# Kernel tuning notes

Hardware: AMD Instinct MI355X
Metric: run time of the kernel (lower is better)

Reference implementation:

```python
import jax, jax.numpy as jnp
import numpy as np

B, T, D_IN, D_OUT = 2, 2048, 2048, 2048
H, KV = 32, 8
HD = D_OUT // H          # 64
G = H // KV              # group_size = 4
ROPE_BASE = 10000.0


def setup_inputs() -> dict:
    key = jax.random.key(0)
    ks = jax.random.split(key, 5)
    s = 0.02  # weight init scale
    return {
        "x":  jax.random.normal(ks[0], (B, T, D_IN), jnp.float32),
        "Wq": jax.random.normal(ks[1], (D_IN, D_OUT), jnp.float32) * s,
        "Wk": jax.random.normal(ks[2], (D_IN, KV * HD), jnp.float32) * s,
        "Wv": jax.random.normal(ks[3], (D_IN, KV * HD), jnp.float32) * s,
        "Wo": jax.random.normal(ks[4], (D_OUT, D_OUT), jnp.float32) * s,
    }


def _rope_cos_sin(t, hd):
    inv = 1.0 / (ROPE_BASE ** (jnp.arange(0, hd, 2, dtype=jnp.float32) / hd))
    ang = jnp.arange(t, dtype=jnp.float32)[:, None] * inv[None, :]  # (T, hd/2)
    return jnp.cos(ang), jnp.sin(ang)


def _apply_rope(x, cos, sin):
    # x: (b, h, T, hd); rotate adjacent pairs (complex multiply, Llama-style)
    xr = x.reshape(x.shape[:-1] + (HD // 2, 2))
    x0, x1 = xr[..., 0], xr[..., 1]
    c = cos[None, None]  # (1,1,T,hd/2)
    s = sin[None, None]
    o0 = x0 * c - x1 * s
    o1 = x0 * s + x1 * c
    return jnp.stack([o0, o1], axis=-1).reshape(x.shape)


def reference(x, Wq, Wk, Wv, Wo):
    b, t, _ = x.shape
    q = (x @ Wq).reshape(b, t, H, HD).transpose(0, 2, 1, 3)    # (b,H,T,hd)
    k = (x @ Wk).reshape(b, t, KV, HD).transpose(0, 2, 1, 3)   # (b,KV,T,hd)
    v = (x @ Wv).reshape(b, t, KV, HD).transpose(0, 2, 1, 3)
    cos, sin = _rope_cos_sin(t, HD)
    q = _apply_rope(q, cos, sin)
    k = _apply_rope(k, cos, sin)
    # GQA: expand KV groups to all heads (repeat_interleave on head dim)
    k = jnp.repeat(k, G, axis=1)  # (b,H,T,hd)
    v = jnp.repeat(v, G, axis=1)
    scores = jnp.einsum('bhqd,bhkd->bhqk', q, k) / jnp.sqrt(jnp.float32(HD))
    causal = jnp.triu(jnp.ones((t, t), dtype=bool), 1)
    scores = jnp.where(causal[None, None], -jnp.inf, scores)
    w = jax.nn.softmax(scores, axis=-1)
    ctx = jnp.einsum('bhqk,bhkd->bqhd', w, v).reshape(b, t, D_OUT)
    return ctx @ Wo
```

## Files before the change

### kernel.cpp

```cpp
#include <hip/hip_runtime.h>

#define TQ 2048
#define NB 2
#define NH 32
#define NKV 8
#define HD 64
#define DIN 2048
#define DOUT 2048
#define NQKV 3072
#define QK_W 2560
#define GK 2048

typedef unsigned short u16;
typedef unsigned int u32;
typedef __attribute__((ext_vector_type(8))) short bf16x8;
typedef __attribute__((ext_vector_type(4))) float f32x4;
typedef __attribute__((ext_vector_type(4))) u16 u16x4;

typedef __attribute__((address_space(1))) const u32 gas_u32;
typedef __attribute__((address_space(3))) u32 las_u32;

#define NEG (-1.0e30f)
#define CL2 0.18033688f

__device__ __forceinline__ u16 f2bf(float f) {
  u32 u = __float_as_uint(f);
  u += 0x7fffu + ((u >> 16) & 1u);
  return (u16)(u >> 16);
}
__device__ __forceinline__ float bf2f(u16 h) { return __uint_as_float(((u32)h) << 16); }
__device__ __forceinline__ u32 cvtpk(float lo, float hi) {
  u32 r;
  asm("v_cvt_pk_bf16_f32 %0, %1, %2" : "=v"(r) : "v"(lo), "v"(hi));
  return r;
}
__device__ __forceinline__ float exp2g(float x) {
  float r;
  asm("v_exp_f32 %0, %1\n\ts_nop 0" : "=v"(r) : "v"(x));
  return r;
}

__global__ __launch_bounds__(256)
void k_cvt(const float* __restrict__ src, u16* __restrict__ dst, int n4) {
  int i = blockIdx.x * 256 + threadIdx.x;
  if (i >= n4) return;
  f32x4 v = *(const f32x4*)(src + (size_t)i * 4);
  u16x4 o;
  o[0] = f2bf(v[0]); o[1] = f2bf(v[1]); o[2] = f2bf(v[2]); o[3] = f2bf(v[3]);
  *(u16x4*)(dst + (size_t)i * 4) = o;
}

__global__ __launch_bounds__(256)
void k_transpose(const float* __restrict__ src, int nsrc, u16* __restrict__ dst, int row0) {
  __shared__ float tile[32][33];
  const int nTK = GK / 32;
  int kt = blockIdx.x % nTK, nt = blockIdx.x / nTK;
  int k0 = kt * 32, n0 = nt * 32;
  int rr = threadIdx.x >> 5, cc = threadIdx.x & 31;
#pragma unroll
  for (int p = 0; p < 4; ++p) {
    int kl = p * 8 + rr;
    tile[kl][cc] = src[(size_t)(k0 + kl) * nsrc + n0 + cc];
  }
  __syncthreads();
#pragma unroll
  for (int p = 0; p < 4; ++p) {
    int nl = p * 8 + rr;
    dst[(size_t)(row0 + n0 + nl) * GK + k0 + cc] = f2bf(tile[cc][nl]);
  }
}

__global__ __launch_bounds__(256)
void k_rope_table(float2* __restrict__ tab) {
  int idx = blockIdx.x * 256 + threadIdx.x;
  int t = idx >> 5, i = idx & 31;
  float inv = 1.0f / powf(10000.0f, (float)i / 32.0f);
  float ang = (float)t * inv;
  tab[idx] = make_float2(cosf(ang), sinf(ang));
}

template <int MODE>
__global__ __launch_bounds__(256, 2)
void k_gemm(const u16* __restrict__ A, const u16* __restrict__ Bt,
            u16* __restrict__ QKV, u16* __restrict__ Vt, float* __restrict__ Cf,
            const float2* __restrict__ tab, int N) {
  __shared__ __align__(16) u16 lds[2][16384];
  const int tid = threadIdx.x;
  const int lane = tid & 63, wid = tid >> 6;
  const int nTN = N >> 7;
  const int tm = blockIdx.x / nTN, tn = blockIdx.x % nTN;
  const int m0 = tm << 7, n0 = tn << 7;
  const int l15 = lane & 15, lg = lane >> 4;
  const int wr = (wid >> 1) << 6, wc = (wid & 1) << 6;

  f32x4 acc[4][4] = {};

  auto stage = [&](int buf, int k0) {
    u16* base = &lds[buf][0];
#pragma unroll
    for (int p = 0; p < 4; ++p) {
      int c = p * 256 + tid;
      int row = c >> 3, kb = c & 7;
      int ksrc = k0 + ((kb ^ (row & 7)) << 3);
      const u16* sA = A + (size_t)(m0 + row) * GK + ksrc;
      __builtin_amdgcn_global_load_lds((gas_u32*)sA, (las_u32*)(base + c * 8), 16, 0, 0);
      const u16* sB = Bt + (size_t)(n0 + row) * GK + ksrc;
      __builtin_amdgcn_global_load_lds((gas_u32*)sB, (las_u32*)(base + 8192 + c * 8), 16, 0, 0);
    }
  };

  auto compute = [&](int buf) {
    const u16* ldsA = &lds[buf][0];
    const u16* ldsB = &lds[buf][8192];
#pragma unroll
    for (int kk = 0; kk < 2; ++kk) {
      bf16x8 af[4], bfr[4];
#pragma unroll
      for (int m = 0; m < 4; ++m) {
        int row = wr + m * 16 + l15;
        int koff = (kk * 32 + lg * 8) ^ ((row & 7) << 3);
        af[m] = *(const bf16x8*)(ldsA + row * 64 + koff);
      }
#pragma unroll
      for (int n = 0; n < 4; ++n) {
        int row = wc + n * 16 + l15;
        int koff = (kk * 32 + lg * 8) ^ ((row & 7) << 3);
        bfr[n] = *(const bf16x8*)(ldsB + row * 64 + koff);
      }
#pragma unroll
      for (int m = 0; m < 4; ++m)
#pragma unroll
        for (int n = 0; n < 4; ++n)
          acc[m][n] = __builtin_amdgcn_mfma_f32_16x16x32_bf16(af[m], bfr[n], acc[m][n], 0, 0, 0);
    }
  };

  stage(0, 0);
  __syncthreads();
  const int nk = GK / 64;
  for (int t = 0; t < nk; ++t) {
    if (t + 1 < nk) stage((t + 1) & 1, (t + 1) * 64);
    compute(t & 1);
    __syncthreads();
  }

  if (MODE == 1) {
#pragma unroll
    for (int m = 0; m < 4; ++m)
#pragma unroll
      for (int n = 0; n < 4; ++n)
#pragma unroll
        for (int r = 0; r < 4; ++r) {
          int row = m0 + wr + m * 16 + lg * 4 + r;
          int col = n0 + wc + n * 16 + l15;
          Cf[(size_t)row * N + col] = acc[m][n][r];
        }
  } else if (n0 >= 2560) {
#pragma unroll
    for (int m = 0; m < 4; ++m)
#pragma unroll
      for (int n = 0; n < 4; ++n)
#pragma unroll
        for (int r = 0; r < 4; ++r) {
          int row = m0 + wr + m * 16 + lg * 4 + r;
          int col = n0 + wc + n * 16 + l15;
          int dh = col - 2560, kvh = dh >> 6, d = dh & 63;
          int bb = row >> 11, tt = row & 2047;
          Vt[(((size_t)bb * NKV + kvh) * 64 + d) * TQ + tt] = f2bf(acc[m][n][r]);
        }
  } else {
#pragma unroll
    for (int m = 0; m < 4; ++m)
#pragma unroll
      for (int n = 0; n < 4; ++n) {
        int col = n0 + wc + n * 16 + l15;
        int dh = (col & 63) >> 1;
        float sgn = (col & 1) ? 1.0f : -1.0f;
#pragma unroll
        for (int r = 0; r < 4; ++r) {
          int row = m0 + wr + m * 16 + lg * 4 + r;
          float a = acc[m][n][r];
          float b = __shfl_xor(a, 1);
          int t = row & (TQ - 1);
          float2 csv = tab[t * 32 + dh];
          float o = a * csv.x + sgn * b * csv.y;
          QKV[(size_t)row * QK_W + col] = f2bf(o);
        }
      }
  }
}

__global__ __launch_bounds__(256, 3)
void k_attn(const u16* __restrict__ QKV, const u16* __restrict__ Vt, u16* __restrict__ ctx) {
  __shared__ __align__(16) u16 Ksh[2][4096];
  __shared__ __align__(16) u16 Vsh[2][4096];
  __shared__ __align__(16) u16 Psh[4][2048];
  const int tid = threadIdx.x, lane = tid & 63, w = tid >> 6;
  const int l15 = lane & 15, lg = lane >> 4;
  const int bid = blockIdx.x;
  const int qt = 15 - (bid >> 6);
  const int hb = bid & 63;
  const int h = hb & 31, b = hb >> 5;
  const int kvh = h >> 2;
  const int q0 = qt << 7;
  const int qb = q0 + w * 32;
  const size_t rowbase = (size_t)b * TQ;
  const u16* Vg = Vt + ((size_t)(b * NKV + kvh)) * 64 * TQ;

  auto stage = [&](int buf, int kv0) {
    u16* kd = &Ksh[buf][0];
    u16* vd = &Vsh[buf][0];
#pragma unroll
    for (int p = 0; p < 2; ++p) {
      int c = p * 256 + tid;
      int row = c >> 3, kb = c & 7;
      int off = (kb ^ (row & 7)) << 3;
      const u16* sK = QKV + (rowbase + kv0 + row) * QK_W + 2048 + kvh * 64 + off;
      __builtin_amdgcn_global_load_lds((gas_u32*)sK, (las_u32*)(kd + c * 8), 16, 0, 0);
      const u16* sV = Vg + (size_t)row * TQ + kv0 + off;
      __builtin_amdgcn_global_load_lds((gas_u32*)sV, (las_u32*)(vd + c * 8), 16, 0, 0);
    }
  };

  bf16x8 qf[2][2];
#pragma unroll
  for (int m = 0; m < 2; ++m)
#pragma unroll
    for (int kk = 0; kk < 2; ++kk)
      qf[m][kk] = *(const bf16x8*)(QKV + (rowbase + qb + m * 16 + l15) * QK_W + h * 64 + kk * 32 + lg * 8);

  float m_run[2] = {NEG, NEG}, l_run[2] = {0.f, 0.f};
  f32x4 oacc[2][4] = {};

  stage(0, 0);
  const int nt = 2 * qt + 2;
  for (int t = 0; t < nt; ++t) {
    const int kv0 = t << 6;
    __syncthreads();
    if (t + 1 < nt) stage((t + 1) & 1, kv0 + 64);
    if (kv0 > qb + 31) continue;

    const u16* Kl = &Ksh[t & 1][0];
    const u16* Vl = &Vsh[t & 1][0];

    f32x4 stv[2][4];
#pragma unroll
    for (int c = 0; c < 4; ++c) {
      const int krow = c * 16 + l15;
      const int ks = (krow & 7) << 3;
      f32x4 z0 = {}, z1 = {};
#pragma unroll
      for (int kk = 0; kk < 2; ++kk) {
        bf16x8 kf = *(const bf16x8*)(Kl + krow * 64 + ((kk * 32 + lg * 8) ^ ks));
        z0 = __builtin_amdgcn_mfma_f32_16x16x32_bf16(kf, qf[0][kk], z0, 0, 0, 0);
        z1 = __builtin_amdgcn_mfma_f32_16x16x32_bf16(kf, qf[1][kk], z1, 0, 0, 0);
      }
      stv[0][c] = z0; stv[1][c] = z1;
    }

    const bool maskT = (kv0 + 63 > qb);
    float mt[2];
    if (maskT) {
#pragma unroll
      for (int m = 0; m < 2; ++m) {
        const int qpos = qb + m * 16 + l15;
        float mx = NEG;
#pragma unroll
        for (int c = 0; c < 4; ++c)
#pragma unroll
          for (int r = 0; r < 4; ++r) {
            int kvpos = kv0 + c * 16 + lg * 4 + r;
            float sv = stv[m][c][r];
            sv = (kvpos > qpos) ? NEG : sv;
            stv[m][c][r] = sv;
            mx = fmaxf(mx, sv);
          }
        mt[m] = mx;
      }
    } else {
#pragma unroll
      for (int m = 0; m < 2; ++m) {
        float mx = NEG;
#pragma unroll
        for (int c = 0; c < 4; ++c)
#pragma unroll
          for (int r = 0; r < 4; ++r) mx = fmaxf(mx, stv[m][c][r]);
        mt[m] = mx;
      }
    }
#pragma unroll
    for (int m = 0; m < 2; ++m) {
      mt[m] = fmaxf(mt[m], __shfl_xor(mt[m], 16));
      mt[m] = fmaxf(mt[m], __shfl_xor(mt[m], 32));
    }

    if (__any((mt[0] > m_run[0] + 64.0f) || (mt[1] > m_run[1] + 64.0f))) {
#pragma unroll
      for (int m = 0; m < 2; ++m) {
        float nm = fmaxf(m_run[m], mt[m]);
        float sc = exp2g((m_run[m] - nm) * CL2);
        m_run[m] = nm;
        l_run[m] *= sc;
#pragma unroll
        for (int dt = 0; dt < 4; ++dt) oacc[m][dt] *= sc;
      }
    }

    u16* Pw = &Psh[w][0];
#pragma unroll
    for (int m = 0; m < 2; ++m) {
      const float msc = m_run[m] * CL2;
      float ssum = 0.f;
      const int rowp = m * 16 + l15;
      const int swz = (l15 & 7) << 3;
#pragma unroll
      for (int c = 0; c < 4; ++c) {
        float p0 = exp2g(stv[m][c][0] * CL2 - msc);
        float p1 = exp2g(stv[m][c][1] * CL2 - msc);
        float p2 = exp2g(stv[m][c][2] * CL2 - msc);
        float p3 = exp2g(stv[m][c][3] * CL2 - msc);
        ssum += (p0 + p1) + (p2 + p3);
        const int kvb = (c * 16 + lg * 4) ^ swz;
        *(u32*)(Pw + rowp * 64 + kvb)       = cvtpk(p0, p1);
        *(u32*)(Pw + rowp * 64 + (kvb | 2)) = cvtpk(p2, p3);
      }
      ssum += __shfl_xor(ssum, 16);
      ssum += __shfl_xor(ssum, 32);
      l_run[m] += ssum;
    }

    bf16x8 pf[2][2];
#pragma unroll
    for (int m = 0; m < 2; ++m)
#pragma unroll
      for (int kc = 0; kc < 2; ++kc)
        pf[m][kc] = *(const bf16x8*)(Pw + (m * 16 + l15) * 64 + ((kc * 32 + lg * 8) ^ ((l15 & 7) << 3)));
#pragma unroll
    for (int dt = 0; dt < 4; ++dt) {
      const int vrow = dt * 16 + l15;
      const int vs = (vrow & 7) << 3;
#pragma unroll
      for (int kc = 0; kc < 2; ++kc) {
        bf16x8 vf = *(const bf16x8*)(Vl + vrow * 64 + ((kc * 32 + lg * 8) ^ vs));
        oacc[0][dt] = __builtin_amdgcn_mfma_f32_16x16x32_bf16(vf, pf[0][kc], oacc[0][dt], 0, 0, 0);
        oacc[1][dt] = __builtin_amdgcn_mfma_f32_16x16x32_bf16(vf, pf[1][kc], oacc[1][dt], 0, 0, 0);
      }
    }
  }

#pragma unroll
  for (int m = 0; m < 2; ++m) {
    float inv = 1.0f / l_run[m];
    size_t row = rowbase + qb + m * 16 + l15;
#pragma unroll
    for (int dt = 0; dt < 4; ++dt) {
      int col = h * 64 + dt * 16 + lg * 4;
      u32 w0 = cvtpk(oacc[m][dt][0] * inv, oacc[m][dt][1] * inv);
      u32 w1 = cvtpk(oacc[m][dt][2] * inv, oacc[m][dt][3] * inv);
      *(u32*)(ctx + row * DOUT + col) = w0;
      *(u32*)(ctx + row * DOUT + col + 2) = w1;
    }
  }
}

extern "C" void kernel_launch(void* const* d_in, const int* in_sizes, int n_in,
                              void* d_out, int out_size, void* d_ws, size_t ws_size,
                              hipStream_t stream) {
  const float* x  = (const float*)d_in[0];
  const float* Wq = (const float*)d_in[1];
  const float* Wk = (const float*)d_in[2];
  const float* Wv = (const float*)d_in[3];
  const float* Wo = (const float*)d_in[4];
  float* out = (float*)d_out;

  char* ws = (char*)d_ws;
  size_t off = 0;
  auto alloc = [&](size_t bytes) -> void* {
    void* p = ws + off;
    off += (bytes + 255) & ~(size_t)255;
    return p;
  };
  const int rows = NB * TQ;
  u16*    xb    = (u16*)alloc((size_t)rows * DIN * 2);
  u16*    WqkvT = (u16*)alloc((size_t)NQKV * GK * 2);
  u16*    WoT   = (u16*)alloc((size_t)DOUT * GK * 2);
  u16*    QKV   = (u16*)alloc((size_t)rows * QK_W * 2);
  u16*    Vt    = (u16*)alloc((size_t)NB * NKV * 64 * TQ * 2);
  u16*    ctx   = (u16*)alloc((size_t)rows * DOUT * 2);
  float2* tab   = (float2*)alloc((size_t)TQ * 32 * sizeof(float2));

  k_cvt<<<dim3(rows * DIN / 4 / 256), dim3(256), 0, stream>>>(x, xb, rows * DIN / 4);
  k_transpose<<<dim3((GK / 32) * (2048 / 32)), dim3(256), 0, stream>>>(Wq, 2048, WqkvT, 0);
  k_transpose<<<dim3((GK / 32) * (512 / 32)),  dim3(256), 0, stream>>>(Wk, 512,  WqkvT, 2048);
  k_transpose<<<dim3((GK / 32) * (512 / 32)),  dim3(256), 0, stream>>>(Wv, 512,  WqkvT, 2560);
  k_transpose<<<dim3((GK / 32) * (2048 / 32)), dim3(256), 0, stream>>>(Wo, 2048, WoT, 0);
  k_rope_table<<<dim3(TQ * 32 / 256), dim3(256), 0, stream>>>(tab);

  k_gemm<0><<<dim3((rows / 128) * (NQKV / 128)), dim3(256), 0, stream>>>(xb, WqkvT, QKV, Vt, nullptr, tab, NQKV);
  k_attn<<<dim3(NB * NH * (TQ / 128)), dim3(256), 0, stream>>>(QKV, Vt, ctx);
  k_gemm<1><<<dim3((rows / 128) * (DOUT / 128)), dim3(256), 0, stream>>>(ctx, WoT, nullptr, nullptr, out, nullptr, DOUT);
}
```

Baseline: 191.9 us.

## Replace QKV GEMM with 256x192 tile, 512-thread kernel and interleaved staging

Adds a dedicated QKV projection kernel using 256x192 block tiles with 8 waves. It launches exactly 256 blocks, one wave of blocks across the GPU, instead of 768 smaller 128x128 blocks. Global-to-LDS loads for the next k-step are split into pieces interleaved with MFMA quads behind raw barriers, and MFMA issue is wrapped in s_setprio. The aim is more operand reuse per LDS load and better overlap of memory and compute. The cost is higher register pressure (96 accumulators per thread) and hand-written waitcnt/barrier ordering that must be correct. The output GEMM is split into its own f32-only kernel.

```diff
diff --git a/kernel.cpp b/kernel.cpp
--- a/kernel.cpp
+++ b/kernel.cpp
@@ -79,11 +79,136 @@
   tab[idx] = make_float2(cosf(ang), sinf(ang));
 }
 
-template <int MODE>
+#define BM2 256
+#define BN2 192
+
+__global__ __launch_bounds__(512, 1)
+void k_gemm256(const u16* __restrict__ A, const u16* __restrict__ Bt,
+               u16* __restrict__ QKV, u16* __restrict__ Vt,
+               const float2* __restrict__ tab) {
+  __shared__ __align__(16) u16 Asl[2][BM2 * 64];
+  __shared__ __align__(16) u16 Bsl[2][BN2 * 64];
+  const int tid = threadIdx.x;
+  const int lane = tid & 63, w = tid >> 6;
+  const int l15 = lane & 15, lg = lane >> 4;
+  const int tm = blockIdx.x >> 4, tn = blockIdx.x & 15;
+  const int m0 = tm * BM2, n0 = tn * BN2;
+  const int wr = w >> 2, wc = w & 3;
+
+  f32x4 acc[8][3] = {};
+
+  auto stageA = [&](int buf, int kt, int half) {
+#pragma unroll
+    for (int i = 0; i < 2; ++i) {
+      int idx = i * 512 + tid;
+      int row = half * 128 + (idx >> 3);
+      int kb = idx & 7;
+      int ksrc = kt * 64 + ((kb ^ (row & 7)) << 3);
+      const u16* s = A + (size_t)(m0 + row) * GK + ksrc;
+      __builtin_amdgcn_global_load_lds((gas_u32*)s,
+          (las_u32*)(&Asl[buf][half * 128 * 64] + idx * 8), 16, 0, 0);
+    }
+  };
+  auto stageB = [&](int buf, int kt) {
+#pragma unroll
+    for (int i = 0; i < 3; ++i) {
+      int idx = i * 512 + tid;
+      int row = idx >> 3;
+      int kb = idx & 7;
+      int ksrc = kt * 64 + ((kb ^ (row & 7)) << 3);
+      const u16* s = Bt + (size_t)(n0 + row) * GK + ksrc;
+      __builtin_amdgcn_global_load_lds((gas_u32*)s,
+          (las_u32*)(&Bsl[buf][0] + idx * 8), 16, 0, 0);
+    }
+  };
+  auto loadB = [&](int buf, int kk, bf16x8* bf) {
+#pragma unroll
+    for (int n = 0; n < 3; ++n) {
+      int row = wc * 48 + n * 16 + l15;
+      int koff = (kk * 32 + lg * 8) ^ ((row & 7) << 3);
+      bf[n] = *(const bf16x8*)(&Bsl[buf][0] + row * 64 + koff);
+    }
+  };
+  auto loadA = [&](int buf, int mh, int kk, bf16x8* af) {
+#pragma unroll
+    for (int mi = 0; mi < 4; ++mi) {
+      int row = wr * 128 + (mh * 4 + mi) * 16 + l15;
+      int koff = (kk * 32 + lg * 8) ^ ((row & 7) << 3);
+      af[mi] = *(const bf16x8*)(&Asl[buf][0] + row * 64 + koff);
+    }
+  };
+  auto quad = [&](int mh, const bf16x8* af, const bf16x8* bf) {
+    __builtin_amdgcn_s_setprio(1);
+#pragma unroll
+    for (int mi = 0; mi < 4; ++mi)
+#pragma unroll
+      for (int n = 0; n < 3; ++n)
+        acc[mh * 4 + mi][n] =
+            __builtin_amdgcn_mfma_f32_16x16x32_bf16(af[mi], bf[n], acc[mh * 4 + mi][n], 0, 0, 0);
+    __builtin_amdgcn_s_setprio(0);
+  };
+
+  stageA(0, 0, 0); stageA(0, 0, 1); stageB(0, 0);
+
+  const int nk = GK / 64;
+  for (int t = 0; t < nk; ++t) {
+    const int buf = t & 1, nb = buf ^ 1;
+    const bool more = (t + 1 < nk);
+    bf16x8 bf0[3], bf1[3], a00[4], a10[4], a01[4], a11[4];
+    if (more) stageA(nb, t + 1, 0);
+    if (more) asm volatile("s_waitcnt vmcnt(2)" ::: "memory");
+    else      asm volatile("s_waitcnt vmcnt(0)" ::: "memory");
+    asm volatile("s_barrier" ::: "memory");
+    loadB(buf, 0, bf0);
+    loadA(buf, 0, 0, a00);
+    quad(0, a00, bf0);
+    if (more) stageA(nb, t + 1, 1);
+    asm volatile("s_barrier" ::: "memory");
+    loadA(buf, 1, 0, a10);
+    quad(1, a10, bf0);
+    if (more) stageB(nb, t + 1);
+    asm volatile("s_barrier" ::: "memory");
+    loadB(buf, 1, bf1);
+    loadA(buf, 0, 1, a01);
+    loadA(buf, 1, 1, a11);
+    quad(0, a01, bf1);
+    asm volatile("s_barrier" ::: "memory");
+    quad(1, a11, bf1);
+  }
+
+#pragma unroll
+  for (int m = 0; m < 8; ++m)
+#pragma unroll
+    for (int n = 0; n < 3; ++n) {
+      int col = n0 + wc * 48 + n * 16 + l15;
+      if (col < 2560) {
+        int dh = (col & 63) >> 1;
+        float sgn = (col & 1) ? 1.0f : -1.0f;
+#pragma unroll
+        for (int r = 0; r < 4; ++r) {
+          int row = m0 + wr * 128 + m * 16 + lg * 4 + r;
+          float a = acc[m][n][r];
+          float b = __shfl_xor(a, 1);
+          int t = row & (TQ - 1);
+          float2 csv = tab[t * 32 + dh];
+          float o = a * csv.x + sgn * b * csv.y;
+          QKV[(size_t)row * QK_W + col] = f2bf(o);
+        }
+      } else {
+        int dh = col - 2560, kvh = dh >> 6, d = dh & 63;
+#pragma unroll
+        for (int r = 0; r < 4; ++r) {
+          int row = m0 + wr * 128 + m * 16 + lg * 4 + r;
+          int bb = row >> 11, tt = row & 2047;
+          Vt[(((size_t)bb * NKV + kvh) * 64 + d) * TQ + tt] = f2bf(acc[m][n][r]);
+        }
+      }
+    }
+}
+
 __global__ __launch_bounds__(256, 2)
-void k_gemm(const u16* __restrict__ A, const u16* __restrict__ Bt,
-            u16* __restrict__ QKV, u16* __restrict__ Vt, float* __restrict__ Cf,
-            const float2* __restrict__ tab, int N) {
+void k_gemm_f32(const u16* __restrict__ A, const u16* __restrict__ Bt,
+                float* __restrict__ Cf, int N) {
   __shared__ __align__(16) u16 lds[2][16384];
   const int tid = threadIdx.x;
   const int lane = tid & 63, wid = tid >> 6;
@@ -144,50 +269,16 @@
     __syncthreads();
   }
 
-  if (MODE == 1) {
-#pragma unroll
-    for (int m = 0; m < 4; ++m)
-#pragma unroll
-      for (int n = 0; n < 4; ++n)
-#pragma unroll
-        for (int r = 0; r < 4; ++r) {
-          int row = m0 + wr + m * 16 + lg * 4 + r;
-          int col = n0 + wc + n * 16 + l15;
-          Cf[(size_t)row * N + col] = acc[m][n][r];
-        }
-  } else if (n0 >= 2560) {
-#pragma unroll
-    for (int m = 0; m < 4; ++m)
-#pragma unroll
-      for (int n = 0; n < 4; ++n)
-#pragma unroll
-        for (int r = 0; r < 4; ++r) {
-          int row = m0 + wr + m * 16 + lg * 4 + r;
-          int col = n0 + wc + n * 16 + l15;
-          int dh = col - 2560, kvh = dh >> 6, d = dh & 63;
-          int bb = row >> 11, tt = row & 2047;
-          Vt[(((size_t)bb * NKV + kvh) * 64 + d) * TQ + tt] = f2bf(acc[m][n][r]);
-        }
-  } else {
-#pragma unroll
-    for (int m = 0; m < 4; ++m)
-#pragma unroll
-      for (int n = 0; n < 4; ++n) {
+#pragma unroll
+  for (int m = 0; m < 4; ++m)
+#pragma unroll
+    for (int n = 0; n < 4; ++n)
+#pragma unroll
+      for (int r = 0; r < 4; ++r) {
+        int row = m0 + wr + m * 16 + lg * 4 + r;
         int col = n0 + wc + n * 16 + l15;
-        int dh = (col & 63) >> 1;
-        float sgn = (col & 1) ? 1.0f : -1.0f;
-#pragma unroll
-        for (int r = 0; r < 4; ++r) {
-          int row = m0 + wr + m * 16 + lg * 4 + r;
-          float a = acc[m][n][r];
-          float b = __shfl_xor(a, 1);
-          int t = row & (TQ - 1);
-          float2 csv = tab[t * 32 + dh];
-          float o = a * csv.x + sgn * b * csv.y;
-          QKV[(size_t)row * QK_W + col] = f2bf(o);
-        }
-      }
-  }
+        Cf[(size_t)row * N + col] = acc[m][n][r];
+      }
 }
 
 __global__ __launch_bounds__(256, 3)
@@ -396,7 +487,7 @@
   k_transpose<<<dim3((GK / 32) * (2048 / 32)), dim3(256), 0, stream>>>(Wo, 2048, WoT, 0);
   k_rope_table<<<dim3(TQ * 32 / 256), dim3(256), 0, stream>>>(tab);
 
-  k_gemm<0><<<dim3((rows / 128) * (NQKV / 128)), dim3(256), 0, stream>>>(xb, WqkvT, QKV, Vt, nullptr, tab, NQKV);
+  k_gemm256<<<dim3(256), dim3(512), 0, stream>>>(xb, WqkvT, QKV, Vt, tab);
   k_attn<<<dim3(NB * NH * (TQ / 128)), dim3(256), 0, stream>>>(QKV, Vt, ctx);
-  k_gemm<1><<<dim3((rows / 128) * (DOUT / 128)), dim3(256), 0, stream>>>(ctx, WoT, nullptr, nullptr, out, nullptr, DOUT);
-}
+  k_gemm_f32<<<dim3((rows / 128) * (DOUT / 128)), dim3(256), 0, stream>>>(ctx, WoT, out, DOUT);
+}
```

Measured after the change: 196.0 us. 1.02x slower.

## Replace QKV projection GEMM with 256x256-tile 8-wave ping-pong pipelined kernel

Applied to the files above, without the earlier changes.

The QKV projection GEMM moves from 128x128 tiles with 4 waves to 256x256 tiles with 8 waves (512 threads). Global-to-LDS loads are interleaved between quarter-tile MFMA phases under explicit vmcnt waits and raw s_barriers, and MFMA priority is raised with setprio. The aim is more data reuse per LDS byte and better overlap of memory traffic with matrix math. The trade-off is a much smaller grid (192 blocks) and higher register pressure. The output projection GEMM is split into its own f32 kernel with unchanged logic.

```diff
diff --git a/kernel.cpp b/kernel.cpp
--- a/kernel.cpp
+++ b/kernel.cpp
@@ -10,6 +10,7 @@
 #define NQKV 3072
 #define QK_W 2560
 #define GK 2048
+#define NKT 32
 
 typedef unsigned short u16;
 typedef unsigned int u32;
@@ -39,6 +40,8 @@
   asm("v_exp_f32 %0, %1\n\ts_nop 0" : "=v"(r) : "v"(x));
   return r;
 }
+
+#define BAR() asm volatile("s_barrier" ::: "memory")
 
 __global__ __launch_bounds__(256)
 void k_cvt(const float* __restrict__ src, u16* __restrict__ dst, int n4) {
@@ -79,11 +82,145 @@
   tab[idx] = make_float2(cosf(ang), sinf(ang));
 }
 
-template <int MODE>
+__global__ __launch_bounds__(512, 2)
+void k_gemm0_8p(const u16* __restrict__ A, const u16* __restrict__ Bt,
+                u16* __restrict__ QKV, u16* __restrict__ Vt,
+                const float2* __restrict__ tab) {
+  __shared__ __align__(16) u16 Asl[2][2][8192];
+  __shared__ __align__(16) u16 Bsl[2][2][8192];
+  const int tid = threadIdx.x;
+  const int lane = tid & 63, w = tid >> 6;
+  const int l15 = lane & 15, lg = lane >> 4;
+  const int tm = blockIdx.x / 12, tn = blockIdx.x % 12;
+  const int m0 = tm * 256, n0 = tn * 256;
+  const int wr = w >> 2, wc = w & 3;
+
+  f32x4 acc[8][4] = {};
+
+  auto stA = [&](int buf, int kt, int half) {
+#pragma unroll
+    for (int i = 0; i < 2; ++i) {
+      int idx = i * 512 + tid;
+      int lrow = idx >> 3, kb = idx & 7;
+      int ksrc = kt * 64 + ((kb ^ (lrow & 7)) << 3);
+      const u16* s = A + (size_t)(m0 + half * 128 + lrow) * GK + ksrc;
+      __builtin_amdgcn_global_load_lds((gas_u32*)s, (las_u32*)(&Asl[buf][half][0] + idx * 8), 16, 0, 0);
+    }
+  };
+  auto stB = [&](int buf, int kt, int half) {
+#pragma unroll
+    for (int i = 0; i < 2; ++i) {
+      int idx = i * 512 + tid;
+      int lrow = idx >> 3, kb = idx & 7;
+      int ksrc = kt * 64 + ((kb ^ (lrow & 7)) << 3);
+      const u16* s = Bt + (size_t)(n0 + half * 128 + lrow) * GK + ksrc;
+      __builtin_amdgcn_global_load_lds((gas_u32*)s, (las_u32*)(&Bsl[buf][half][0] + idx * 8), 16, 0, 0);
+    }
+  };
+  auto rdA = [&](int buf, int mh, bf16x8* af) {
+#pragma unroll
+    for (int mi = 0; mi < 4; ++mi) {
+      int lrow = mh * 64 + mi * 16 + l15;
+      int sw = (lrow & 7) << 3;
+#pragma unroll
+      for (int kk = 0; kk < 2; ++kk)
+        af[mi * 2 + kk] = *(const bf16x8*)(&Asl[buf][wr][0] + lrow * 64 + ((kk * 32 + lg * 8) ^ sw));
+    }
+  };
+  auto rdB = [&](int buf, int nh, bf16x8* bf) {
+#pragma unroll
+    for (int n = 0; n < 2; ++n) {
+      int gr = wc * 64 + nh * 32 + n * 16 + l15;
+      int half = gr >> 7, lrow = gr & 127;
+      int sw = (lrow & 7) << 3;
+#pragma unroll
+      for (int kk = 0; kk < 2; ++kk)
+        bf[n * 2 + kk] = *(const bf16x8*)(&Bsl[buf][half][0] + lrow * 64 + ((kk * 32 + lg * 8) ^ sw));
+    }
+  };
+  auto mmaQ = [&](int mh, int nh, const bf16x8* af, const bf16x8* bf) {
+    __builtin_amdgcn_s_setprio(1);
+#pragma unroll
+    for (int mi = 0; mi < 4; ++mi)
+#pragma unroll
+      for (int n = 0; n < 2; ++n)
+#pragma unroll
+        for (int kk = 0; kk < 2; ++kk)
+          acc[mh * 4 + mi][nh * 2 + n] = __builtin_amdgcn_mfma_f32_16x16x32_bf16(
+              af[mi * 2 + kk], bf[n * 2 + kk], acc[mh * 4 + mi][nh * 2 + n], 0, 0, 0);
+    __builtin_amdgcn_s_setprio(0);
+  };
+
+  stB(0, 0, 0); stB(0, 0, 1); stA(0, 0, 0); stA(0, 0, 1);
+  stB(1, 1, 0); stB(1, 1, 1); stA(1, 1, 0); stA(1, 1, 1);
+
+  bf16x8 a0[8], a1[8], b0[4], b1[4];
+  for (int it = 0; it < NKT / 2; ++it) {
+    const int S0 = 2 * it + 2, S1 = 2 * it + 3;
+    const bool st = (S0 < NKT), st2 = (S1 < NKT);
+    asm volatile("s_waitcnt vmcnt(8)" ::: "memory");
+    BAR();
+    rdA(0, 0, a0); rdB(0, 0, b0);
+    mmaQ(0, 0, a0, b0); BAR();
+    rdB(0, 1, b1);
+    BAR(); mmaQ(0, 1, a0, b1); BAR();
+    rdA(0, 1, a1);
+    if (st) stB(0, S0, 0);
+    BAR(); mmaQ(1, 0, a1, b0); BAR();
+    if (st) stB(0, S0, 1);
+    BAR(); mmaQ(1, 1, a1, b1); BAR();
+    if (st) {
+      stA(0, S0, 0);
+      asm volatile("s_waitcnt vmcnt(6)" ::: "memory");
+    } else {
+      asm volatile("s_waitcnt vmcnt(0)" ::: "memory");
+    }
+    BAR();
+    rdA(1, 0, a0); rdB(1, 0, b0);
+    mmaQ(0, 0, a0, b0); BAR();
+    rdB(1, 1, b1);
+    if (st) stA(0, S0, 1);
+    BAR(); mmaQ(0, 1, a0, b1); BAR();
+    rdA(1, 1, a1);
+    if (st2) { stB(1, S1, 0); stB(1, S1, 1); }
+    BAR(); mmaQ(1, 0, a1, b0); BAR();
+    if (st2) { stA(1, S1, 0); stA(1, S1, 1); }
+    BAR(); mmaQ(1, 1, a1, b1); BAR();
+  }
+
+#pragma unroll
+  for (int mf = 0; mf < 8; ++mf)
+#pragma unroll
+    for (int nf = 0; nf < 4; ++nf) {
+      int col = n0 + wc * 64 + nf * 16 + l15;
+      if (col < 2560) {
+        int dh = (col & 63) >> 1;
+        float sgn = (col & 1) ? 1.0f : -1.0f;
+#pragma unroll
+        for (int r = 0; r < 4; ++r) {
+          int row = m0 + wr * 128 + mf * 16 + lg * 4 + r;
+          float a = acc[mf][nf][r];
+          float b = __shfl_xor(a, 1);
+          int t = row & (TQ - 1);
+          float2 csv = tab[t * 32 + dh];
+          float o = a * csv.x + sgn * b * csv.y;
+          QKV[(size_t)row * QK_W + col] = f2bf(o);
+        }
+      } else {
+        int dh = col - 2560, kvh = dh >> 6, d = dh & 63;
+#pragma unroll
+        for (int r = 0; r < 4; ++r) {
+          int row = m0 + wr * 128 + mf * 16 + lg * 4 + r;
+          int bb = row >> 11, tt = row & 2047;
+          Vt[(((size_t)bb * NKV + kvh) * 64 + d) * TQ + tt] = f2bf(acc[mf][nf][r]);
+        }
+      }
+    }
+}
+
 __global__ __launch_bounds__(256, 2)
-void k_gemm(const u16* __restrict__ A, const u16* __restrict__ Bt,
-            u16* __restrict__ QKV, u16* __restrict__ Vt, float* __restrict__ Cf,
-            const float2* __restrict__ tab, int N) {
+void k_gemm_f32(const u16* __restrict__ A, const u16* __restrict__ Bt,
+                float* __restrict__ Cf, int N) {
   __shared__ __align__(16) u16 lds[2][16384];
   const int tid = threadIdx.x;
   const int lane = tid & 63, wid = tid >> 6;
@@ -144,50 +281,16 @@
     __syncthreads();
   }
 
-  if (MODE == 1) {
-#pragma unroll
-    for (int m = 0; m < 4; ++m)
-#pragma unroll
-      for (int n = 0; n < 4; ++n)
-#pragma unroll
-        for (int r = 0; r < 4; ++r) {
-          int row = m0 + wr + m * 16 + lg * 4 + r;
-          int col = n0 + wc + n * 16 + l15;
-          Cf[(size_t)row * N + col] = acc[m][n][r];
-        }
-  } else if (n0 >= 2560) {
-#pragma unroll
-    for (int m = 0; m < 4; ++m)
-#pragma unroll
-      for (int n = 0; n < 4; ++n)
-#pragma unroll
-        for (int r = 0; r < 4; ++r) {
-          int row = m0 + wr + m * 16 + lg * 4 + r;
-          int col = n0 + wc + n * 16 + l15;
-          int dh = col - 2560, kvh = dh >> 6, d = dh & 63;
-          int bb = row >> 11, tt = row & 2047;
-          Vt[(((size_t)bb * NKV + kvh) * 64 + d) * TQ + tt] = f2bf(acc[m][n][r]);
-        }
-  } else {
-#pragma unroll
-    for (int m = 0; m < 4; ++m)
-#pragma unroll
-      for (int n = 0; n < 4; ++n) {
+#pragma unroll
+  for (int m = 0; m < 4; ++m)
+#pragma unroll
+    for (int n = 0; n < 4; ++n)
+#pragma unroll
+      for (int r = 0; r < 4; ++r) {
+        int row = m0 + wr + m * 16 + lg * 4 + r;
         int col = n0 + wc + n * 16 + l15;
-        int dh = (col & 63) >> 1;
-        float sgn = (col & 1) ? 1.0f : -1.0f;
-#pragma unroll
-        for (int r = 0; r < 4; ++r) {
-          int row = m0 + wr + m * 16 + lg * 4 + r;
-          float a = acc[m][n][r];
-          float b = __shfl_xor(a, 1);
-          int t = row & (TQ - 1);
-          float2 csv = tab[t * 32 + dh];
-          float o = a * csv.x + sgn * b * csv.y;
-          QKV[(size_t)row * QK_W + col] = f2bf(o);
-        }
-      }
-  }
+        Cf[(size_t)row * N + col] = acc[m][n][r];
+      }
 }
 
 __global__ __launch_bounds__(256, 3)
@@ -396,7 +499,7 @@
   k_transpose<<<dim3((GK / 32) * (2048 / 32)), dim3(256), 0, stream>>>(Wo, 2048, WoT, 0);
   k_rope_table<<<dim3(TQ * 32 / 256), dim3(256), 0, stream>>>(tab);
 
-  k_gemm<0><<<dim3((rows / 128) * (NQKV / 128)), dim3(256), 0, stream>>>(xb, WqkvT, QKV, Vt, nullptr, tab, NQKV);
+  k_gemm0_8p<<<dim3(16 * 12), dim3(512), 0, stream>>>(xb, WqkvT, QKV, Vt, tab);
   k_attn<<<dim3(NB * NH * (TQ / 128)), dim3(256), 0, stream>>>(QKV, Vt, ctx);
-  k_gemm<1><<<dim3((rows / 128) * (DOUT / 128)), dim3(256), 0, stream>>>(ctx, WoT, nullptr, nullptr, out, nullptr, DOUT);
-}
+  k_gemm_f32<<<dim3((rows / 128) * (DOUT / 128)), dim3(256), 0, stream>>>(ctx, WoT, out, DOUT);
+}
```

After: 190.7 us. No clear change (-0.6%).
